# Optimization experiments

Measured on AMD Instinct MI355X. Metric: run time of the kernel, lower is better.

The kernel has to match this reference:

```python
import jax, jax.numpy as jnp
import numpy as np

N = 20000
E = 320000
DIN = 256
DH = 64
DOUT = 64
H = 8
NEG_SLOPE = 0.2


def _glorot(key, shape):
    fan_in, fan_out = shape[0], shape[-1]
    lim = jnp.sqrt(6.0 / (fan_in + fan_out))
    return jax.random.uniform(key, shape, jnp.float32, -lim, lim)


def setup_inputs() -> dict:
    key = jax.random.key(0)
    ks = jax.random.split(key, 12)
    x = jax.random.normal(ks[0], (N, DIN), jnp.float32)
    edge_index = jax.random.randint(ks[1], (2, E), 0, N, jnp.int32)
    # layer 1: dim_in -> heads*dim_h
    Wl1 = _glorot(ks[2], (DIN, H * DH));  bl1 = jnp.zeros((H * DH,), jnp.float32)
    Wr1 = _glorot(ks[3], (DIN, H * DH));  br1 = jnp.zeros((H * DH,), jnp.float32)
    att1 = _glorot(ks[4], (H, DH))
    bias1 = jnp.zeros((H * DH,), jnp.float32)
    # layer 2: heads*dim_h -> heads*dim_out
    Wl2 = _glorot(ks[5], (H * DH, H * DOUT)); bl2 = jnp.zeros((H * DOUT,), jnp.float32)
    Wr2 = _glorot(ks[6], (H * DH, H * DOUT)); br2 = jnp.zeros((H * DOUT,), jnp.float32)
    att2 = _glorot(ks[7], (H, DOUT))
    bias2 = jnp.zeros((H * DOUT,), jnp.float32)
    return dict(x=x, edge_index=edge_index, Wl1=Wl1, bl1=bl1, Wr1=Wr1, br1=br1,
                att1=att1, bias1=bias1, Wl2=Wl2, bl2=bl2, Wr2=Wr2, br2=br2,
                att2=att2, bias2=bias2)


def _gatv2(x, src, dst, Wl, bl, Wr, br, att, bias_out, heads, out_ch):
    n = x.shape[0]
    l = (x @ Wl + bl).reshape(n, heads, out_ch)   # source transform
    r = (x @ Wr + br).reshape(n, heads, out_ch)   # target transform
    # per-edge GATv2 score: att . LeakyReLU(l_j + r_i)
    e = jax.nn.leaky_relu(l[src] + r[dst], NEG_SLOPE)      # [E, H, C]
    logits = jnp.einsum('ehc,hc->eh', e, att)              # [E, H]
    # segmented softmax over incoming edges of each destination node
    m = jax.ops.segment_max(logits, dst, num_segments=n)   # [N, H]
    expd = jnp.exp(logits - m[dst])
    denom = jax.ops.segment_sum(expd, dst, num_segments=n)
    alpha = expd / denom[dst]                              # [E, H]
    msg = l[src] * alpha[:, :, None]                       # [E, H, C]
    out = jax.ops.segment_sum(msg, dst, num_segments=n)    # [N, H, C]
    return out.reshape(n, heads * out_ch) + bias_out


def reference(x, edge_index, Wl1, bl1, Wr1, br1, att1, bias1,
              Wl2, bl2, Wr2, br2, att2, bias2):
    n = x.shape[0]
    loops = jnp.arange(n, dtype=edge_index.dtype)
    src = jnp.concatenate([edge_index[0], loops])  # GATv2Conv adds self-loops
    dst = jnp.concatenate([edge_index[1], loops])
    # dropout is identity at inference
    h = _gatv2(x, src, dst, Wl1, bl1, Wr1, br1, att1, bias1, H, DH)
    h = jax.nn.elu(h)
    h = _gatv2(h, src, dst, Wl2, bl2, Wr2, br2, att2, bias2, H, DOUT)
    return h, jax.nn.log_softmax(h, axis=1)
```

## Files before the change

### kernel.cpp

```cpp
#include <hip/hip_runtime.h>
#include <math.h>

#define NN   20000
#define NE   320000
#define ET   (NE + NN)
#define CPAD 16
#define D_IN 256
#define DHID 512
#define NLR  1024
#define MPAD 20096
#define NROWP 157
#define NCOLP 8

typedef __attribute__((ext_vector_type(8))) short bf16x8;
typedef __attribute__((ext_vector_type(4))) float f32x4;

typedef __attribute__((address_space(3))) uint       lds_uint;
typedef __attribute__((address_space(1))) const uint gbl_uint;
#define ASYNC16(gp, lp) \
    __builtin_amdgcn_global_load_lds((gbl_uint*)(gp), (lds_uint*)(lp), 16, 0, 0)

__device__ __forceinline__ ushort f2bf(float f) {
    uint u = __float_as_uint(f);
    return (ushort)((u + 0x7fffu + ((u >> 16) & 1u)) >> 16);
}


__global__ __launch_bounds__(256) void init_count(int* count, int* csr_src) {
    int i = blockIdx.x * 256 + threadIdx.x;
    if (i < NN) count[i] = 1;
    if (i < CPAD) csr_src[ET + i] = 0;
}

__global__ __launch_bounds__(256) void hist_kernel(const int* __restrict__ dstv,
                                                   int* __restrict__ count) {
    int e = blockIdx.x * 256 + threadIdx.x;
    if (e < NE) atomicAdd(&count[dstv[e]], 1);
}

__global__ __launch_bounds__(1024) void scan_kernel(const int* __restrict__ count,
                                                    int* __restrict__ offs,
                                                    int* __restrict__ cursor) {
    __shared__ int sm[1024];
    const int CH = 20;
    int t = threadIdx.x;
    int base = t * CH;
    int local[CH];
    int s = 0;
#pragma unroll
    for (int i = 0; i < CH; i++) {
        int idx = base + i;
        int v = (idx < NN) ? count[idx] : 0;
        local[i] = s;
        s += v;
    }
    sm[t] = s;
    __syncthreads();
    for (int o = 1; o < 1024; o <<= 1) {
        int v = (t >= o) ? sm[t - o] : 0;
        __syncthreads();
        sm[t] += v;
        __syncthreads();
    }
    int pref = (t > 0) ? sm[t - 1] : 0;
#pragma unroll
    for (int i = 0; i < CH; i++) {
        int idx = base + i;
        if (idx < NN) {
            int o_ = pref + local[i];
            offs[idx] = o_;
            cursor[idx] = o_;
        }
    }
    if (t == 1023) offs[NN] = sm[1023];
}

__global__ __launch_bounds__(256) void scatter_kernel(const int* __restrict__ srcv,
                                                      const int* __restrict__ dstv,
                                                      int* __restrict__ cursor,
                                                      int* __restrict__ csr_src) {
    int e = blockIdx.x * 256 + threadIdx.x;
    if (e >= ET) return;
    int s, d;
    if (e < NE) { s = srcv[e]; d = dstv[e]; }
    else        { s = e - NE;  d = s; }
    int pos = atomicAdd(&cursor[d], 1);
    csr_src[pos] = s;
}


#define N1Q ((long)MPAD * D_IN / 4)
#define N2Q ((long)(MPAD - NN) * DHID / 4)

__global__ __launch_bounds__(256) void prep_a(const float* __restrict__ x,
                                              ushort* __restrict__ a) {
    long t = (long)blockIdx.x * 256 + threadIdx.x;
    if (t < N1Q) {
        long e = t * 4;
        int row = (int)(e >> 8);
        float4 v = make_float4(0.f, 0.f, 0.f, 0.f);
        if (row < NN) v = *(const float4*)&x[e];
        ushort4 o;
        o.x = f2bf(v.x); o.y = f2bf(v.y); o.z = f2bf(v.z); o.w = f2bf(v.w);
        *(ushort4*)&a[e] = o;
    } else if (t < N1Q + N2Q) {
        long e = (t - N1Q) * 4 + (long)NN * DHID;
        ushort4 z = {0, 0, 0, 0};
        *(ushort4*)&a[e] = z;
    }
}


__global__ __launch_bounds__(256) void transpose_w2(const float* __restrict__ Wl1,
                                                    const float* __restrict__ Wr1,
                                                    ushort* __restrict__ Wt1,
                                                    const float* __restrict__ Wl2,
                                                    const float* __restrict__ Wr2,
                                                    ushort* __restrict__ Wt2) {
    __shared__ float tile[32][33];
    int z = blockIdx.z;
    int K = z ? DHID : D_IN;
    int k0 = blockIdx.x * 32;
    if (k0 >= K) return;
    int n0 = blockIdx.y * 32;
    int tx = threadIdx.x & 31, ty = threadIdx.x >> 5;
    const float* __restrict__ W = (n0 < DHID) ? (z ? Wl2 : Wl1) : (z ? Wr2 : Wr1);
    ushort* __restrict__ Wt = z ? Wt2 : Wt1;
    int nb = (n0 < DHID) ? n0 : n0 - DHID;
#pragma unroll
    for (int r = ty; r < 32; r += 8)
        tile[r][tx] = W[(long)(k0 + r) * DHID + nb + tx];
    __syncthreads();
#pragma unroll
    for (int r = ty; r < 32; r += 8)
        Wt[(long)(n0 + r) * K + k0 + tx] = f2bf(tile[tx][r]);
}


#define BM 128
#define BN 128
#define BK 64

__global__ __launch_bounds__(256) void gemm_mfma(const ushort* __restrict__ A, int K,
                                                 const ushort* __restrict__ Wt,
                                                 const float* __restrict__ bl,
                                                 const float* __restrict__ br,
                                                 ushort* __restrict__ out) {
    __shared__ ushort As[BM * BK];
    __shared__ ushort Bs[BN * BK];

    int t = threadIdx.x;
    int bid = blockIdx.x;
    int xcd = bid & 7;
    int idx = bid >> 3;
    int gl = xcd * NROWP + idx;
    int row0 = (gl >> 3) * BM;
    int col0 = (gl & 7) * BN;

    int lane = t & 63, w = t >> 6;
    int wr = w >> 1, wc = w & 1;
    int l16 = lane & 15, lhi = lane >> 4;

    f32x4 acc[4][4];
#pragma unroll
    for (int m = 0; m < 4; m++)
#pragma unroll
        for (int n = 0; n < 4; n++)
            acc[m][n] = (f32x4){0.f, 0.f, 0.f, 0.f};

    for (int k0 = 0; k0 < K; k0 += BK) {
#pragma unroll
        for (int q = 0; q < 4; q++) {
            int chunk = q * 256 + t;
            int row = chunk >> 3;
            int il = (chunk & 7) ^ (row & 7);
            ASYNC16(A  + (long)(row0 + row) * K + k0 + il * 8, (char*)As + chunk * 16);
            ASYNC16(Wt + (long)(col0 + row) * K + k0 + il * 8, (char*)Bs + chunk * 16);
        }
        __syncthreads();
#pragma unroll
        for (int kk = 0; kk < 2; kk++) {
            bf16x8 af[4], bfr[4];
#pragma unroll
            for (int m = 0; m < 4; m++) {
                int rl = wr * 64 + m * 16 + l16;
                int off = rl * 128 + ((kk * 64 + lhi * 16) ^ ((rl & 7) << 4));
                af[m] = *(const bf16x8*)((const char*)As + off);
            }
#pragma unroll
            for (int n = 0; n < 4; n++) {
                int rl = wc * 64 + n * 16 + l16;
                int off = rl * 128 + ((kk * 64 + lhi * 16) ^ ((rl & 7) << 4));
                bfr[n] = *(const bf16x8*)((const char*)Bs + off);
            }
#pragma unroll
            for (int m = 0; m < 4; m++)
#pragma unroll
                for (int n = 0; n < 4; n++)
                    acc[m][n] = __builtin_amdgcn_mfma_f32_16x16x32_bf16(bfr[n], af[m], acc[m][n], 0, 0, 0);
        }
        __syncthreads();
    }

    float4 bvn[4];
#pragma unroll
    for (int n = 0; n < 4; n++) {
        int colb = col0 + wc * 64 + n * 16 + lhi * 4;
        bvn[n] = (colb < DHID) ? *(const float4*)&bl[colb]
                               : *(const float4*)&br[colb - DHID];
    }
#pragma unroll
    for (int m = 0; m < 4; m++) {
        int row = row0 + wr * 64 + m * 16 + l16;
        if (row < NN) {
#pragma unroll
            for (int n = 0; n < 4; n++) {
                int colb = col0 + wc * 64 + n * 16 + lhi * 4;
                ushort4 p;
                p.x = f2bf(acc[m][n][0] + bvn[n].x);
                p.y = f2bf(acc[m][n][1] + bvn[n].y);
                p.z = f2bf(acc[m][n][2] + bvn[n].z);
                p.w = f2bf(acc[m][n][3] + bvn[n].w);
                *(ushort4*)&out[(long)row * NLR + colb] = p;
            }
        }
    }
}


#define CVT8(u, f)                                  \
    f[0] = __uint_as_float((u).x << 16);            \
    f[1] = __uint_as_float((u).x & 0xffff0000u);    \
    f[2] = __uint_as_float((u).y << 16);            \
    f[3] = __uint_as_float((u).y & 0xffff0000u);    \
    f[4] = __uint_as_float((u).z << 16);            \
    f[5] = __uint_as_float((u).z & 0xffff0000u);    \
    f[6] = __uint_as_float((u).w << 16);            \
    f[7] = __uint_as_float((u).w & 0xffff0000u);

template <int MODE>
__global__ __launch_bounds__(256) void aggregate_kernel(const ushort* __restrict__ lr,
                                                        const float* __restrict__ att,
                                                        const float* __restrict__ bias,
                                                        const int* __restrict__ csr_src,
                                                        const int* __restrict__ offs,
                                                        ushort* __restrict__ out_bf,
                                                        float* __restrict__ out_f32,
                                                        float* __restrict__ out_lsm) {
    int i = blockIdx.x * 4 + (threadIdx.x >> 6);
    int lane = threadIdx.x & 63;
    int c0 = lane << 3;

    uint4 ur = *(const uint4*)(lr + (long)i * NLR + DHID + c0);
    float rv[8];
    CVT8(ur, rv);
    float av[8];
    *(float4*)&av[0] = *(const float4*)&att[c0];
    *(float4*)&av[4] = *(const float4*)&att[c0 + 4];

    int beg = offs[i], end = offs[i + 1];
    float m = -3.0e38f, d = 0.f;
    float acc[8] = {0.f, 0.f, 0.f, 0.f, 0.f, 0.f, 0.f, 0.f};

    int j = csr_src[beg];
    uint4 v = *(const uint4*)(lr + (long)j * NLR + c0);

    for (int k = beg; k < end; k++) {
        uint4 vc = v;
        int kn = (k + 1 < end) ? k + 1 : k;
        int jn = csr_src[kn];
        v = *(const uint4*)(lr + (long)jn * NLR + c0);

        float lx[8];
        CVT8(vc, lx);
        float s = 0.f;
#pragma unroll
        for (int c = 0; c < 8; c++) {
            float e = lx[c] + rv[c];
            e = fmaxf(e, 0.2f * e);
            s = fmaf(av[c], e, s);
        }
        s *= 1.44269504f;
        s += __shfl_xor(s, 1);
        s += __shfl_xor(s, 2);
        s += __shfl_xor(s, 4);

        if (s > m) {
            float sc = exp2f(m - s);
            d *= sc;
#pragma unroll
            for (int c = 0; c < 8; c++) acc[c] *= sc;
            m = s;
        }
        float wgt = exp2f(s - m);
        d += wgt;
#pragma unroll
        for (int c = 0; c < 8; c++) acc[c] = fmaf(wgt, lx[c], acc[c]);
    }

    float inv = 1.f / d;
    float o[8];
    float4 bi0 = *(const float4*)&bias[c0];
    float4 bi1 = *(const float4*)&bias[c0 + 4];
    o[0] = fmaf(acc[0], inv, bi0.x); o[1] = fmaf(acc[1], inv, bi0.y);
    o[2] = fmaf(acc[2], inv, bi0.z); o[3] = fmaf(acc[3], inv, bi0.w);
    o[4] = fmaf(acc[4], inv, bi1.x); o[5] = fmaf(acc[5], inv, bi1.y);
    o[6] = fmaf(acc[6], inv, bi1.z); o[7] = fmaf(acc[7], inv, bi1.w);

    if (MODE == 0) {
#pragma unroll
        for (int c = 0; c < 8; c++) o[c] = (o[c] > 0.f) ? o[c] : expm1f(o[c]);
        uint4 p;
        p.x = (uint)f2bf(o[0]) | ((uint)f2bf(o[1]) << 16);
        p.y = (uint)f2bf(o[2]) | ((uint)f2bf(o[3]) << 16);
        p.z = (uint)f2bf(o[4]) | ((uint)f2bf(o[5]) << 16);
        p.w = (uint)f2bf(o[6]) | ((uint)f2bf(o[7]) << 16);
        *(uint4*)(out_bf + (long)i * DHID + c0) = p;
    } else {
        *(float4*)&out_f32[(long)i * DHID + c0]     = *(float4*)&o[0];
        *(float4*)&out_f32[(long)i * DHID + c0 + 4] = *(float4*)&o[4];
        float mx = o[0];
#pragma unroll
        for (int c = 1; c < 8; c++) mx = fmaxf(mx, o[c]);
#pragma unroll
        for (int off = 1; off < 64; off <<= 1) mx = fmaxf(mx, __shfl_xor(mx, off));
        float se = 0.f;
#pragma unroll
        for (int c = 0; c < 8; c++) se += __expf(o[c] - mx);
#pragma unroll
        for (int off = 1; off < 64; off <<= 1) se += __shfl_xor(se, off);
        float lg = mx + logf(se);
        float l0[8];
#pragma unroll
        for (int c = 0; c < 8; c++) l0[c] = o[c] - lg;
        *(float4*)&out_lsm[(long)i * DHID + c0]     = *(float4*)&l0[0];
        *(float4*)&out_lsm[(long)i * DHID + c0 + 4] = *(float4*)&l0[4];
    }
}


extern "C" void kernel_launch(void* const* d_in, const int* in_sizes, int n_in,
                              void* d_out, int out_size, void* d_ws, size_t ws_size,
                              hipStream_t stream) {
    const float* x     = (const float*)d_in[0];
    const int*   ei    = (const int*)d_in[1];
    const float* Wl1   = (const float*)d_in[2];
    const float* bl1   = (const float*)d_in[3];
    const float* Wr1   = (const float*)d_in[4];
    const float* br1   = (const float*)d_in[5];
    const float* att1  = (const float*)d_in[6];
    const float* bias1 = (const float*)d_in[7];
    const float* Wl2   = (const float*)d_in[8];
    const float* bl2   = (const float*)d_in[9];
    const float* Wr2   = (const float*)d_in[10];
    const float* br2   = (const float*)d_in[11];
    const float* att2  = (const float*)d_in[12];
    const float* bias2 = (const float*)d_in[13];

    float* out = (float*)d_out;
    float* h2  = out;
    float* lsm = out + (long)NN * DHID;

    ushort* lrbuf  = (ushort*)d_ws;
    ushort* Abf    = lrbuf + (long)NN * NLR;
    ushort* Wt1    = Abf + (long)MPAD * DHID;
    ushort* Wt2    = Wt1 + (long)NLR * D_IN;
    int*    csr_src = (int*)(Wt2 + (long)NLR * DHID);
    int*    count   = csr_src + ET + CPAD;
    int*    offs    = count + NN;
    int*    cursor  = offs + NN + 1;

    const int* srcv = ei;
    const int* dstv = ei + NE;

    prep_a<<<(int)((N1Q + N2Q + 255) / 256), 256, 0, stream>>>(x, Abf);
    transpose_w2<<<dim3(DHID / 32, NLR / 32, 2), 256, 0, stream>>>(Wl1, Wr1, Wt1,
                                                                   Wl2, Wr2, Wt2);

    init_count<<<(NN + 255) / 256, 256, 0, stream>>>(count, csr_src);
    hist_kernel<<<(NE + 255) / 256, 256, 0, stream>>>(dstv, count);
    scan_kernel<<<1, 1024, 0, stream>>>(count, offs, cursor);
    scatter_kernel<<<(ET + 255) / 256, 256, 0, stream>>>(srcv, dstv, cursor, csr_src);

    gemm_mfma<<<NROWP * NCOLP, 256, 0, stream>>>(Abf, D_IN, Wt1, bl1, br1, lrbuf);
    aggregate_kernel<0><<<NN / 4, 256, 0, stream>>>(lrbuf, att1, bias1, csr_src, offs, Abf, nullptr, nullptr);

    gemm_mfma<<<NROWP * NCOLP, 256, 0, stream>>>(Abf, DHID, Wt2, bl2, br2, lrbuf);
    aggregate_kernel<1><<<NN / 4, 256, 0, stream>>>(lrbuf, att2, bias2, csr_src, offs, nullptr, h2, lsm);
}
```

Baseline: 262.6 us.

## Merge independent setup kernels into combined launches to cut launch count

Independent kernels are packed into shared launches that dispatch on block index: the input bf16 prep runs with the count init, the degree histogram with the weight transpose, and the CSR scatter with the first GEMM. The launch count drops from ten to seven, which removes launch gaps and lets unrelated work overlap on the device. In exchange, the scatter blocks take on the GEMM kernel's large LDS allocation, which may limit their occupancy, and the GEMM block-to-tile mapping depends on GEMM blocks staying at the low block indices.

```diff
diff --git a/kernel.cpp b/kernel.cpp
--- a/kernel.cpp
+++ b/kernel.cpp
@@ -26,17 +26,77 @@
 }
 
 
-__global__ __launch_bounds__(256) void init_count(int* count, int* csr_src) {
-    int i = blockIdx.x * 256 + threadIdx.x;
-    if (i < NN) count[i] = 1;
-    if (i < CPAD) csr_src[ET + i] = 0;
-}
-
-__global__ __launch_bounds__(256) void hist_kernel(const int* __restrict__ dstv,
-                                                   int* __restrict__ count) {
-    int e = blockIdx.x * 256 + threadIdx.x;
-    if (e < NE) atomicAdd(&count[dstv[e]], 1);
-}
+#define N1Q ((long)MPAD * D_IN / 4)
+#define N2Q ((long)(MPAD - NN) * DHID / 4)
+#define PREP_BLKS ((int)((N1Q + N2Q + 255) / 256))
+#define INIT_BLKS ((NN + 255) / 256)
+
+__global__ __launch_bounds__(256) void k_prep(const float* __restrict__ x,
+                                              ushort* __restrict__ a,
+                                              int* __restrict__ count,
+                                              int* __restrict__ csr_src) {
+    int b = blockIdx.x;
+    if (b < PREP_BLKS) {
+        long t = (long)b * 256 + threadIdx.x;
+        if (t < N1Q) {
+            long e = t * 4;
+            int row = (int)(e >> 8);
+            float4 v = make_float4(0.f, 0.f, 0.f, 0.f);
+            if (row < NN) v = *(const float4*)&x[e];
+            ushort4 o;
+            o.x = f2bf(v.x); o.y = f2bf(v.y); o.z = f2bf(v.z); o.w = f2bf(v.w);
+            *(ushort4*)&a[e] = o;
+        } else if (t < N1Q + N2Q) {
+            long e = (t - N1Q) * 4 + (long)NN * DHID;
+            ushort4 z = {0, 0, 0, 0};
+            *(ushort4*)&a[e] = z;
+        }
+    } else {
+        int i = (b - PREP_BLKS) * 256 + threadIdx.x;
+        if (i < NN) count[i] = 1;
+        if (i < CPAD) csr_src[ET + i] = 0;
+    }
+}
+
+
+#define HIST_BLKS ((NE + 255) / 256)
+#define TW_BLKS   1024
+
+__global__ __launch_bounds__(256) void k_hist_tw(const int* __restrict__ dstv,
+                                                 int* __restrict__ count,
+                                                 const float* __restrict__ Wl1,
+                                                 const float* __restrict__ Wr1,
+                                                 ushort* __restrict__ Wt1,
+                                                 const float* __restrict__ Wl2,
+                                                 const float* __restrict__ Wr2,
+                                                 ushort* __restrict__ Wt2) {
+    __shared__ float tile[32][33];
+    int b = blockIdx.x;
+    if (b < HIST_BLKS) {
+        int e = b * 256 + threadIdx.x;
+        if (e < NE) atomicAdd(&count[dstv[e]], 1);
+        return;
+    }
+    int idx = b - HIST_BLKS;
+    int z = idx >> 9;
+    int rem = idx & 511;
+    int K = z ? DHID : D_IN;
+    int k0 = (rem & 15) * 32;
+    if (k0 >= K) return;
+    int n0 = (rem >> 4) * 32;
+    int tx = threadIdx.x & 31, ty = threadIdx.x >> 5;
+    const float* __restrict__ W = (n0 < DHID) ? (z ? Wl2 : Wl1) : (z ? Wr2 : Wr1);
+    ushort* __restrict__ Wt = z ? Wt2 : Wt1;
+    int nb = (n0 < DHID) ? n0 : n0 - DHID;
+#pragma unroll
+    for (int r = ty; r < 32; r += 8)
+        tile[r][tx] = W[(long)(k0 + r) * DHID + nb + tx];
+    __syncthreads();
+#pragma unroll
+    for (int r = ty; r < 32; r += 8)
+        Wt[(long)(n0 + r) * K + k0 + tx] = f2bf(tile[tx][r]);
+}
+
 
 __global__ __launch_bounds__(1024) void scan_kernel(const int* __restrict__ count,
                                                     int* __restrict__ offs,
@@ -75,82 +135,38 @@
     if (t == 1023) offs[NN] = sm[1023];
 }
 
-__global__ __launch_bounds__(256) void scatter_kernel(const int* __restrict__ srcv,
+
+#define BM 128
+#define BN 128
+#define BK 64
+#define GEMM_BLKS (NROWP * NCOLP)
+#define SCAT_BLKS ((ET + 255) / 256)
+
+__global__ __launch_bounds__(256) void k_gemm_scatter(const ushort* __restrict__ A, int K,
+                                                      const ushort* __restrict__ Wt,
+                                                      const float* __restrict__ bl,
+                                                      const float* __restrict__ br,
+                                                      ushort* __restrict__ out,
+                                                      const int* __restrict__ srcv,
                                                       const int* __restrict__ dstv,
                                                       int* __restrict__ cursor,
                                                       int* __restrict__ csr_src) {
-    int e = blockIdx.x * 256 + threadIdx.x;
-    if (e >= ET) return;
-    int s, d;
-    if (e < NE) { s = srcv[e]; d = dstv[e]; }
-    else        { s = e - NE;  d = s; }
-    int pos = atomicAdd(&cursor[d], 1);
-    csr_src[pos] = s;
-}
-
-
-#define N1Q ((long)MPAD * D_IN / 4)
-#define N2Q ((long)(MPAD - NN) * DHID / 4)
-
-__global__ __launch_bounds__(256) void prep_a(const float* __restrict__ x,
-                                              ushort* __restrict__ a) {
-    long t = (long)blockIdx.x * 256 + threadIdx.x;
-    if (t < N1Q) {
-        long e = t * 4;
-        int row = (int)(e >> 8);
-        float4 v = make_float4(0.f, 0.f, 0.f, 0.f);
-        if (row < NN) v = *(const float4*)&x[e];
-        ushort4 o;
-        o.x = f2bf(v.x); o.y = f2bf(v.y); o.z = f2bf(v.z); o.w = f2bf(v.w);
-        *(ushort4*)&a[e] = o;
-    } else if (t < N1Q + N2Q) {
-        long e = (t - N1Q) * 4 + (long)NN * DHID;
-        ushort4 z = {0, 0, 0, 0};
-        *(ushort4*)&a[e] = z;
-    }
-}
-
-
-__global__ __launch_bounds__(256) void transpose_w2(const float* __restrict__ Wl1,
-                                                    const float* __restrict__ Wr1,
-                                                    ushort* __restrict__ Wt1,
-                                                    const float* __restrict__ Wl2,
-                                                    const float* __restrict__ Wr2,
-                                                    ushort* __restrict__ Wt2) {
-    __shared__ float tile[32][33];
-    int z = blockIdx.z;
-    int K = z ? DHID : D_IN;
-    int k0 = blockIdx.x * 32;
-    if (k0 >= K) return;
-    int n0 = blockIdx.y * 32;
-    int tx = threadIdx.x & 31, ty = threadIdx.x >> 5;
-    const float* __restrict__ W = (n0 < DHID) ? (z ? Wl2 : Wl1) : (z ? Wr2 : Wr1);
-    ushort* __restrict__ Wt = z ? Wt2 : Wt1;
-    int nb = (n0 < DHID) ? n0 : n0 - DHID;
-#pragma unroll
-    for (int r = ty; r < 32; r += 8)
-        tile[r][tx] = W[(long)(k0 + r) * DHID + nb + tx];
-    __syncthreads();
-#pragma unroll
-    for (int r = ty; r < 32; r += 8)
-        Wt[(long)(n0 + r) * K + k0 + tx] = f2bf(tile[tx][r]);
-}
-
-
-#define BM 128
-#define BN 128
-#define BK 64
-
-__global__ __launch_bounds__(256) void gemm_mfma(const ushort* __restrict__ A, int K,
-                                                 const ushort* __restrict__ Wt,
-                                                 const float* __restrict__ bl,
-                                                 const float* __restrict__ br,
-                                                 ushort* __restrict__ out) {
     __shared__ ushort As[BM * BK];
     __shared__ ushort Bs[BN * BK];
 
+    int bid = blockIdx.x;
+    if (bid >= GEMM_BLKS) {
+        int e = (bid - GEMM_BLKS) * 256 + threadIdx.x;
+        if (e >= ET) return;
+        int s, d;
+        if (e < NE) { s = srcv[e]; d = dstv[e]; }
+        else        { s = e - NE;  d = s; }
+        int pos = atomicAdd(&cursor[d], 1);
+        csr_src[pos] = s;
+        return;
+    }
+
     int t = threadIdx.x;
-    int bid = blockIdx.x;
     int xcd = bid & 7;
     int idx = bid >> 3;
     int gl = xcd * NROWP + idx;
@@ -373,18 +389,16 @@
     const int* srcv = ei;
     const int* dstv = ei + NE;
 
-    prep_a<<<(int)((N1Q + N2Q + 255) / 256), 256, 0, stream>>>(x, Abf);
-    transpose_w2<<<dim3(DHID / 32, NLR / 32, 2), 256, 0, stream>>>(Wl1, Wr1, Wt1,
-                                                                   Wl2, Wr2, Wt2);
-
-    init_count<<<(NN + 255) / 256, 256, 0, stream>>>(count, csr_src);
-    hist_kernel<<<(NE + 255) / 256, 256, 0, stream>>>(dstv, count);
+    k_prep<<<PREP_BLKS + INIT_BLKS, 256, 0, stream>>>(x, Abf, count, csr_src);
+    k_hist_tw<<<HIST_BLKS + TW_BLKS, 256, 0, stream>>>(dstv, count, Wl1, Wr1, Wt1,
+                                                       Wl2, Wr2, Wt2);
     scan_kernel<<<1, 1024, 0, stream>>>(count, offs, cursor);
-    scatter_kernel<<<(ET + 255) / 256, 256, 0, stream>>>(srcv, dstv, cursor, csr_src);
-
-    gemm_mfma<<<NROWP * NCOLP, 256, 0, stream>>>(Abf, D_IN, Wt1, bl1, br1, lrbuf);
+
+    k_gemm_scatter<<<GEMM_BLKS + SCAT_BLKS, 256, 0, stream>>>(Abf, D_IN, Wt1, bl1, br1,
+                                                              lrbuf, srcv, dstv, cursor, csr_src);
     aggregate_kernel<0><<<NN / 4, 256, 0, stream>>>(lrbuf, att1, bias1, csr_src, offs, Abf, nullptr, nullptr);
 
-    gemm_mfma<<<NROWP * NCOLP, 256, 0, stream>>>(Abf, DHID, Wt2, bl2, br2, lrbuf);
+    k_gemm_scatter<<<GEMM_BLKS, 256, 0, stream>>>(Abf, DHID, Wt2, bl2, br2,
+                                                  lrbuf, nullptr, nullptr, nullptr, nullptr);
     aggregate_kernel<1><<<NN / 4, 256, 0, stream>>>(lrbuf, att2, bias2, csr_src, offs, nullptr, h2, lsm);
 }
```

Measured after the change: 254.7 us. 1.03x faster.
